# Optimization experiments

Hardware: AMD Instinct MI355X
Metric: run time of the kernel (lower is better)

## Reference

```python
import jax, jax.numpy as jnp
import numpy as np
from jax import lax

WINDOW_SIZE = 11
SIGMA = 1.5
LEVELS = 5
WEIGHTS = jnp.array([0.0448, 0.2856, 0.3001, 0.2363, 0.1333], dtype=jnp.float32)


def _make_window(ws, channel):
    # 1D gaussian, sigma=1.5, normalized; outer product -> 2D window, tiled per channel
    x = jnp.arange(ws, dtype=jnp.float32) - ws // 2
    g = jnp.exp(-(x * x) / (2.0 * SIGMA * SIGMA))
    g = g / g.sum()
    w2 = jnp.outer(g, g)  # [ws, ws]
    return jnp.broadcast_to(w2[None, None], (channel, 1, ws, ws))


def _dwconv(x, win, channel):
    # depthwise VALID conv, matches F.conv2d(..., padding=0, groups=channel)
    return lax.conv_general_dilated(
        x, win, window_strides=(1, 1), padding='VALID',
        feature_group_count=channel,
        dimension_numbers=('NCHW', 'OIHW', 'NCHW'))


def _ssim_cs(img1, img2):
    # dynamic data range, as in the torch source (L=1 for [0,1) inputs)
    max_val = jnp.where(jnp.max(img1) > 128.0, 255.0, 1.0)
    min_val = jnp.where(jnp.min(img1) < -0.5, -1.0, 0.0)
    L = max_val - min_val

    n, c, h, w = img1.shape
    ws = min(WINDOW_SIZE, h, w)  # static python int
    win = _make_window(ws, c)

    mu1 = _dwconv(img1, win, c)
    mu2 = _dwconv(img2, win, c)
    mu1_sq = mu1 * mu1
    mu2_sq = mu2 * mu2
    mu1_mu2 = mu1 * mu2
    sigma1_sq = _dwconv(img1 * img1, win, c) - mu1_sq
    sigma2_sq = _dwconv(img2 * img2, win, c) - mu2_sq
    sigma12 = _dwconv(img1 * img2, win, c) - mu1_mu2

    C1 = (0.01 * L) ** 2
    C2 = (0.03 * L) ** 2
    v1 = 2.0 * sigma12 + C2
    v2 = sigma1_sq + sigma2_sq + C2
    cs = jnp.mean(v1 / v2)
    ssim_map = (2.0 * mu1_mu2 + C1) * v1 / ((mu1_sq + mu2_sq + C1) * v2)
    return jnp.mean(ssim_map), cs


def _avg_pool2(x):
    # F.avg_pool2d(x, (2,2)): stride 2, no padding (floors odd dims)
    n, c, h, w = x.shape
    x = x[:, :, : (h // 2) * 2, : (w // 2) * 2]
    return x.reshape(n, c, h // 2, 2, w // 2, 2).mean(axis=(3, 5))


def setup_inputs() -> dict:
    key = jax.random.key(0)
    k1, k2 = jax.random.split(key)
    img1 = jax.random.uniform(k1, (16, 3, 512, 512), dtype=jnp.float32)
    img2 = jax.random.uniform(k2, (16, 3, 512, 512), dtype=jnp.float32)
    return {"img1": img1, "img2": img2}


def reference(img1, img2):
    mssim, mcs = [], []
    for _ in range(LEVELS):  # fixed 5-level pyramid, shapes shrink each level
        s, c = _ssim_cs(img1, img2)
        mssim.append(s)
        mcs.append(c)
        img1 = _avg_pool2(img1)
        img2 = _avg_pool2(img2)
    mssim = (jnp.stack(mssim) + 1.0) / 2.0  # normalize=True
    mcs = (jnp.stack(mcs) + 1.0) / 2.0
    pow1 = mcs ** WEIGHTS
    pow2 = mssim ** WEIGHTS
    # NOTE: faithful to source: prod over (pow1[:-1] * pow2[-1]) broadcasts pow2[-1]
    return jnp.prod(pow1[:-1] * pow2[-1])
```

## Files before the change

### kernel.cpp

```cpp
#include <hip/hip_runtime.h>


#define NSLOT 32

typedef float v4  __attribute__((ext_vector_type(4)));
typedef float v2f __attribute__((ext_vector_type(2)));
typedef _Float16 h4 __attribute__((ext_vector_type(4)));

__device__ __forceinline__ float frcp(float x) { return __builtin_amdgcn_rcpf(x); }

template<int TROWS, int NTHR, int MINW>
__global__ __launch_bounds__(NTHR, MINW) void ssim_tile_kernel(
    const float* __restrict__ img1, const float* __restrict__ img2,
    float* __restrict__ ds1, float* __restrict__ ds2,
    int H, int do_ds, float* __restrict__ acc)
{
    constexpr int HR    = TROWS + 10;
    constexpr int OPT   = TROWS * 32 / NTHR;
    constexpr int PITCH = 33;
    constexpr int NW    = NTHR / 64;

    const float GW[11] = {0.00102840f, 0.00759877f, 0.03600070f, 0.10936069f,
                          0.21300636f, 0.26601172f, 0.21300636f, 0.10936069f,
                          0.03600070f, 0.00759877f, 0.00102840f};
    const float C1 = 1e-4f, C2 = 9e-4f;

    __shared__ h4 hb[HR * PITCH];
    __shared__ float red[2 * NW];

    const int tid  = threadIdx.x;
    const int nc   = blockIdx.z;
    const int tx0  = blockIdx.x * 32;
    const int ty0  = blockIdx.y * TROWS;
    const int outHW = H - 10;
    const float* p1 = img1 + (size_t)nc * H * H;
    const float* p2 = img2 + (size_t)nc * H * H;

    if (do_ds) {
        const int H2 = H >> 1;
        #pragma unroll
        for (int t = tid; t < 16 * (TROWS / 2); t += NTHR) {
            int r = t >> 4, cdd = t & 15;
            int iy = ty0 + 2 * r, ix = tx0 + 2 * cdd;
            if (iy + 1 < H) {
                v2f a0 = *(const v2f*)(p1 + (size_t)iy * H + ix);
                v2f a1 = *(const v2f*)(p1 + (size_t)(iy + 1) * H + ix);
                v2f b0 = *(const v2f*)(p2 + (size_t)iy * H + ix);
                v2f b1 = *(const v2f*)(p2 + (size_t)(iy + 1) * H + ix);
                size_t o = (size_t)nc * H2 * H2
                         + (size_t)((ty0 >> 1) + r) * H2 + ((tx0 >> 1) + cdd);
                ds1[o] = 0.25f * ((a0.x + a0.y) + (a1.x + a1.y));
                ds2[o] = 0.25f * ((b0.x + b0.y) + (b1.x + b1.y));
            }
        }
    }

    for (int task = tid; task < HR * 8; task += NTHR) {
        const int r  = task >> 3, cg = task & 7;
        const int gr = ty0 + r;
        const int c0 = tx0 + cg * 4;
        v4 hs = 0.f, hd = 0.f, hss = 0.f, hdd = 0.f;
        if (gr < H) {
            float s[16], d[16];
            if (c0 + 16 <= H) {
                const float* pa = p1 + (size_t)gr * H + c0;
                const float* pb = p2 + (size_t)gr * H + c0;
                #pragma unroll
                for (int q = 0; q < 4; ++q) {
                    v4 va = *(const v4*)(pa + 4 * q);
                    v4 vb = *(const v4*)(pb + 4 * q);
                    v4 sv = va + vb, dv = va - vb;
                    s[4*q+0] = sv.x; s[4*q+1] = sv.y; s[4*q+2] = sv.z; s[4*q+3] = sv.w;
                    d[4*q+0] = dv.x; d[4*q+1] = dv.y; d[4*q+2] = dv.z; d[4*q+3] = dv.w;
                }
            } else {
                #pragma unroll
                for (int q = 0; q < 16; ++q) {
                    int cc = c0 + q;
                    float a = (cc < H) ? p1[(size_t)gr * H + cc] : 0.f;
                    float b = (cc < H) ? p2[(size_t)gr * H + cc] : 0.f;
                    s[q] = a + b; d[q] = a - b;
                }
            }
            #pragma unroll
            for (int j = 0; j < 11; ++j) {
                float w = GW[j];
                v4 sv = {s[j], s[j+1], s[j+2], s[j+3]};
                v4 dv = {d[j], d[j+1], d[j+2], d[j+3]};
                v4 ws = w * sv, wd = w * dv;
                hs += ws; hd += wd; hss += ws * sv; hdd += wd * dv;
            }
        }
        h4* row = &hb[r * PITCH + cg * 4];
        row[0] = (h4){(_Float16)hs.x, (_Float16)hd.x, (_Float16)hss.x, (_Float16)hdd.x};
        row[1] = (h4){(_Float16)hs.y, (_Float16)hd.y, (_Float16)hss.y, (_Float16)hdd.y};
        row[2] = (h4){(_Float16)hs.z, (_Float16)hd.z, (_Float16)hss.z, (_Float16)hdd.z};
        row[3] = (h4){(_Float16)hs.w, (_Float16)hd.w, (_Float16)hss.w, (_Float16)hdd.w};
    }
    __syncthreads();

    const int col  = tid & 31;
    const int row0 = (tid >> 5) * OPT;
    const float colm = (tx0 + col < outHW) ? 1.f : 0.f;
    v4 A[OPT];
    #pragma unroll
    for (int k = 0; k < OPT; ++k) A[k] = 0.f;

    #pragma unroll
    for (int r = 0; r < OPT + 10; ++r) {
        h4 h = hb[(row0 + r) * PITCH + col];
        v4 f = {(float)h.x, (float)h.y, (float)h.z, (float)h.w};
        #pragma unroll
        for (int k = 0; k < OPT; ++k) {
            const int j = r - k;
            if (j >= 0 && j < 11) A[k] += GW[j] * f;
        }
    }

    float ssim_t = 0.f, cs_t = 0.f;
    #pragma unroll
    for (int k = 0; k < OPT; ++k) {
        float mask = colm * ((ty0 + row0 + k < outHW) ? 1.f : 0.f);
        float mu_s = A[k].x, mu_d = A[k].y;
        float P = mu_s * mu_s, Q = mu_d * mu_d;
        float U = A[k].z - P, V = A[k].w - Q;
        float v1 = 0.5f * (U - V) + C2;
        float v2 = 0.5f * (U + V) + C2;
        float n1 = 0.5f * (P - Q) + C1;
        float d1 = 0.5f * (P + Q) + C1;
        float csv = v1 * frcp(v2);
        float ssv = n1 * csv * frcp(d1);
        cs_t   += mask * csv;
        ssim_t += mask * ssv;
    }

    #pragma unroll
    for (int off = 32; off > 0; off >>= 1) {
        ssim_t += __shfl_down(ssim_t, off);
        cs_t   += __shfl_down(cs_t, off);
    }
    int wave = tid >> 6, lane = tid & 63;
    if (lane == 0) { red[wave] = ssim_t; red[NW + wave] = cs_t; }
    __syncthreads();
    if (tid == 0) {
        float s = 0.f, c2s = 0.f;
        #pragma unroll
        for (int w = 0; w < NW; ++w) { s += red[w]; c2s += red[NW + w]; }
        int slot = (blockIdx.x + blockIdx.y * 5 + blockIdx.z * 11) & (NSLOT - 1);
        atomicAdd(&acc[slot], s);
        atomicAdd(&acc[NSLOT + slot], c2s);
    }
}

__global__ void finalize_kernel(const float* __restrict__ acc, float* __restrict__ out)
{
    if (threadIdx.x == 0 && blockIdx.x == 0) {
        const float w[5] = {0.0448f, 0.2856f, 0.3001f, 0.2363f, 0.1333f};
        float ms[5], mc[5];
        for (int l = 0; l < 5; ++l) {
            float s = 0.f, c = 0.f;
            for (int k = 0; k < NSLOT; ++k) {
                s += acc[2 * NSLOT * l + k];
                c += acc[2 * NSLOT * l + NSLOT + k];
            }
            int oh = (512 >> l) - 10;
            float cnt = 48.f * (float)oh * (float)oh;
            ms[l] = (s / cnt + 1.f) * 0.5f;
            mc[l] = (c / cnt + 1.f) * 0.5f;
        }
        float p2 = powf(ms[4], w[4]);
        float r = 1.f;
        for (int i = 0; i < 4; ++i) r *= powf(mc[i], w[i]) * p2;
        out[0] = r;
    }
}

extern "C" void kernel_launch(void* const* d_in, const int* in_sizes, int n_in,
                              void* d_out, int out_size, void* d_ws, size_t ws_size,
                              hipStream_t stream)
{
    const float* img1 = (const float*)d_in[0];
    const float* img2 = (const float*)d_in[1];
    float* out = (float*)d_out;
    float* ws  = (float*)d_ws;

    float* acc = ws;
    size_t off = 512;

    const float* buf1[5];
    const float* buf2[5];
    float* wbuf1[5];
    float* wbuf2[5];
    buf1[0] = img1; buf2[0] = img2;
    for (int l = 1; l < 5; ++l) {
        int Hl = 512 >> l;
        size_t sz = (size_t)48 * Hl * Hl;
        wbuf1[l] = ws + off; off += sz;
        wbuf2[l] = ws + off; off += sz;
        buf1[l] = wbuf1[l];
        buf2[l] = wbuf2[l];
    }

    hipMemsetAsync(acc, 0, 5 * 2 * NSLOT * sizeof(float), stream);

    const int Hs[5] = {512, 256, 128, 64, 32};
    const int Ts[5] = {64, 64, 32, 16, 16};

    for (int l = 0; l < 5; ++l) {
        int H = Hs[l], T = Ts[l];
        int outH = H - 10;
        int ctiles = (outH + 31) / 32;
        int rtiles = (outH + T - 1) / T;
        dim3 grid(ctiles, rtiles, 48);
        float* d1 = l < 4 ? wbuf1[l + 1] : nullptr;
        float* d2 = l < 4 ? wbuf2[l + 1] : nullptr;
        int dd = l < 4 ? 1 : 0;
        float* a = acc + 2 * NSLOT * l;
        if (T == 64)
            ssim_tile_kernel<64, 256, 8><<<grid, 256, 0, stream>>>(buf1[l], buf2[l], d1, d2, H, dd, a);
        else if (T == 32)
            ssim_tile_kernel<32, 256, 8><<<grid, 256, 0, stream>>>(buf1[l], buf2[l], d1, d2, H, dd, a);
        else
            ssim_tile_kernel<16, 256, 8><<<grid, 256, 0, stream>>>(buf1[l], buf2[l], d1, d2, H, dd, a);
    }

    finalize_kernel<<<1, 64, 0, stream>>>(acc, out);
}
```

Measured before the change: 253.2 us.

## Fuse all pyramid levels into one cooperative persistent kernel with grid syncs

Replaces the per-level kernel launches, memset and finalize launch with a single cooperative kernel that loops over tiles for each level and separates levels with grid-wide syncs. Accumulator zeroing and the final combine run inside the same kernel. This aims to remove launch gaps and tail effects between small levels, at the cost of grid sync overhead and occupancy capped by cooperative launch limits; the launch bounds also change from 8 to 4 minimum waves. A fallback path keeps separate launches if cooperative launch fails.

```diff
diff --git a/kernel.cpp b/kernel.cpp
--- a/kernel.cpp
+++ b/kernel.cpp
@@ -1,7 +1,10 @@
 #include <hip/hip_runtime.h>
+#include <hip/hip_cooperative_groups.h>
 
 
 #define NSLOT 32
+
+namespace cg = cooperative_groups;
 
 typedef float v4  __attribute__((ext_vector_type(4)));
 typedef float v2f __attribute__((ext_vector_type(2)));
@@ -9,29 +12,22 @@
 
 __device__ __forceinline__ float frcp(float x) { return __builtin_amdgcn_rcpf(x); }
 
-template<int TROWS, int NTHR, int MINW>
-__global__ __launch_bounds__(NTHR, MINW) void ssim_tile_kernel(
+template<int TROWS>
+__device__ __forceinline__ void ssim_tile(
     const float* __restrict__ img1, const float* __restrict__ img2,
     float* __restrict__ ds1, float* __restrict__ ds2,
-    int H, int do_ds, float* __restrict__ acc)
+    int H, int do_ds, float* __restrict__ acc,
+    int nc, int tx0, int ty0, h4* hb, float* red, int tid)
 {
     constexpr int HR    = TROWS + 10;
-    constexpr int OPT   = TROWS * 32 / NTHR;
+    constexpr int OPT   = TROWS * 32 / 256;
     constexpr int PITCH = 33;
-    constexpr int NW    = NTHR / 64;
 
     const float GW[11] = {0.00102840f, 0.00759877f, 0.03600070f, 0.10936069f,
                           0.21300636f, 0.26601172f, 0.21300636f, 0.10936069f,
                           0.03600070f, 0.00759877f, 0.00102840f};
     const float C1 = 1e-4f, C2 = 9e-4f;
 
-    __shared__ h4 hb[HR * PITCH];
-    __shared__ float red[2 * NW];
-
-    const int tid  = threadIdx.x;
-    const int nc   = blockIdx.z;
-    const int tx0  = blockIdx.x * 32;
-    const int ty0  = blockIdx.y * TROWS;
     const int outHW = H - 10;
     const float* p1 = img1 + (size_t)nc * H * H;
     const float* p2 = img2 + (size_t)nc * H * H;
@@ -39,7 +35,7 @@
     if (do_ds) {
         const int H2 = H >> 1;
         #pragma unroll
-        for (int t = tid; t < 16 * (TROWS / 2); t += NTHR) {
+        for (int t = tid; t < 16 * (TROWS / 2); t += 256) {
             int r = t >> 4, cdd = t & 15;
             int iy = ty0 + 2 * r, ix = tx0 + 2 * cdd;
             if (iy + 1 < H) {
@@ -55,10 +51,10 @@
         }
     }
 
-    for (int task = tid; task < HR * 8; task += NTHR) {
-        const int r  = task >> 3, cg = task & 7;
+    for (int task = tid; task < HR * 8; task += 256) {
+        const int r  = task >> 3, cg_ = task & 7;
         const int gr = ty0 + r;
-        const int c0 = tx0 + cg * 4;
+        const int c0 = tx0 + cg_ * 4;
         v4 hs = 0.f, hd = 0.f, hss = 0.f, hdd = 0.f;
         if (gr < H) {
             float s[16], d[16];
@@ -87,11 +83,11 @@
                 float w = GW[j];
                 v4 sv = {s[j], s[j+1], s[j+2], s[j+3]};
                 v4 dv = {d[j], d[j+1], d[j+2], d[j+3]};
-                v4 ws = w * sv, wd = w * dv;
-                hs += ws; hd += wd; hss += ws * sv; hdd += wd * dv;
+                v4 ws_ = w * sv, wd = w * dv;
+                hs += ws_; hd += wd; hss += ws_ * sv; hdd += wd * dv;
             }
         }
-        h4* row = &hb[r * PITCH + cg * 4];
+        h4* row = &hb[r * PITCH + cg_ * 4];
         row[0] = (h4){(_Float16)hs.x, (_Float16)hd.x, (_Float16)hss.x, (_Float16)hdd.x};
         row[1] = (h4){(_Float16)hs.y, (_Float16)hd.y, (_Float16)hss.y, (_Float16)hdd.y};
         row[2] = (h4){(_Float16)hs.z, (_Float16)hd.z, (_Float16)hss.z, (_Float16)hdd.z};
@@ -140,39 +136,117 @@
         cs_t   += __shfl_down(cs_t, off);
     }
     int wave = tid >> 6, lane = tid & 63;
-    if (lane == 0) { red[wave] = ssim_t; red[NW + wave] = cs_t; }
+    if (lane == 0) { red[wave] = ssim_t; red[4 + wave] = cs_t; }
     __syncthreads();
     if (tid == 0) {
-        float s = 0.f, c2s = 0.f;
-        #pragma unroll
-        for (int w = 0; w < NW; ++w) { s += red[w]; c2s += red[NW + w]; }
-        int slot = (blockIdx.x + blockIdx.y * 5 + blockIdx.z * 11) & (NSLOT - 1);
+        float s = red[0] + red[1] + red[2] + red[3];
+        float c2s = red[4] + red[5] + red[6] + red[7];
+        int slot = (tx0 + ty0 * 5 + nc * 11) & (NSLOT - 1);
         atomicAdd(&acc[slot], s);
         atomicAdd(&acc[NSLOT + slot], c2s);
     }
 }
 
+__device__ __forceinline__ void finalize_body(const float* __restrict__ acc,
+                                              float* __restrict__ out)
+{
+    const float w[5] = {0.0448f, 0.2856f, 0.3001f, 0.2363f, 0.1333f};
+    float ms[5], mc[5];
+    for (int l = 0; l < 5; ++l) {
+        float s = 0.f, c = 0.f;
+        for (int k = 0; k < NSLOT; ++k) {
+            s += acc[2 * NSLOT * l + k];
+            c += acc[2 * NSLOT * l + NSLOT + k];
+        }
+        int oh = (512 >> l) - 10;
+        float cnt = 48.f * (float)oh * (float)oh;
+        ms[l] = (s / cnt + 1.f) * 0.5f;
+        mc[l] = (c / cnt + 1.f) * 0.5f;
+    }
+    float p2 = powf(ms[4], w[4]);
+    float r = 1.f;
+    for (int i = 0; i < 4; ++i) r *= powf(mc[i], w[i]) * p2;
+    out[0] = r;
+}
+
+
+__global__ __launch_bounds__(256, 4) void ssim_all_kernel(
+    const float* __restrict__ img1, const float* __restrict__ img2,
+    float* __restrict__ ws, float* __restrict__ out)
+{
+    __shared__ h4 hb[74 * 33];
+    __shared__ float red[8];
+
+    const int tid = threadIdx.x;
+    const int bid = blockIdx.x;
+    const int nb  = gridDim.x;
+    cg::grid_group grid = cg::this_grid();
+
+    float* acc = ws;
+    float* l1a = ws + 512;      float* l1b = ws + 3146240;
+    float* l2a = ws + 6291968;  float* l2b = ws + 7078400;
+    float* l3a = ws + 7864832;  float* l3b = ws + 8061440;
+    float* l4a = ws + 8258048;  float* l4b = ws + 8307200;
+
+    if (bid == 0)
+        for (int i = tid; i < 2 * NSLOT * 5; i += 256) acc[i] = 0.f;
+    grid.sync();
+
+    for (int t = bid; t < 6144; t += nb) {
+        int nc = t >> 7, k = t & 127;
+        ssim_tile<64>(img1, img2, l1a, l1b, 512, 1, acc,
+                      nc, (k & 15) * 32, (k >> 4) * 64, hb, red, tid);
+    }
+    grid.sync();
+
+    for (int t = bid; t < 1536; t += nb) {
+        int nc = t >> 5, k = t & 31;
+        ssim_tile<64>(l1a, l1b, l2a, l2b, 256, 1, acc + 64,
+                      nc, (k & 7) * 32, (k >> 3) * 64, hb, red, tid);
+    }
+    grid.sync();
+
+    for (int t = bid; t < 768; t += nb) {
+        int nc = t >> 4, k = t & 15;
+        ssim_tile<32>(l2a, l2b, l3a, l3b, 128, 1, acc + 128,
+                      nc, (k & 3) * 32, (k >> 2) * 32, hb, red, tid);
+    }
+    grid.sync();
+
+    for (int t = bid; t < 384; t += nb) {
+        int nc = t >> 3, k = t & 7;
+        ssim_tile<16>(l3a, l3b, l4a, l4b, 64, 1, acc + 192,
+                      nc, (k & 1) * 32, (k >> 1) * 16, hb, red, tid);
+    }
+    grid.sync();
+
+    for (int t = bid; t < 96; t += nb) {
+        int nc = t >> 1, k = t & 1;
+        ssim_tile<16>(l4a, l4b, nullptr, nullptr, 32, 0, acc + 256,
+                      nc, 0, k * 16, hb, red, tid);
+    }
+    grid.sync();
+
+    if (bid == 0 && tid == 0) finalize_body(acc, out);
+}
+
+
+template<int TROWS>
+__global__ __launch_bounds__(256, 4) void ssim_level_kernel(
+    const float* __restrict__ img1, const float* __restrict__ img2,
+    float* __restrict__ ds1, float* __restrict__ ds2,
+    int H, int do_ds, float* __restrict__ acc)
+{
+    __shared__ h4 hb[(TROWS + 10) * 33];
+    __shared__ float red[8];
+    ssim_tile<TROWS>(img1, img2, ds1, ds2, H, do_ds, acc,
+                     blockIdx.z, blockIdx.x * 32, blockIdx.y * TROWS,
+                     hb, red, threadIdx.x);
+}
+
 __global__ void finalize_kernel(const float* __restrict__ acc, float* __restrict__ out)
 {
-    if (threadIdx.x == 0 && blockIdx.x == 0) {
-        const float w[5] = {0.0448f, 0.2856f, 0.3001f, 0.2363f, 0.1333f};
-        float ms[5], mc[5];
-        for (int l = 0; l < 5; ++l) {
-            float s = 0.f, c = 0.f;
-            for (int k = 0; k < NSLOT; ++k) {
-                s += acc[2 * NSLOT * l + k];
-                c += acc[2 * NSLOT * l + NSLOT + k];
-            }
-            int oh = (512 >> l) - 10;
-            float cnt = 48.f * (float)oh * (float)oh;
-            ms[l] = (s / cnt + 1.f) * 0.5f;
-            mc[l] = (c / cnt + 1.f) * 0.5f;
-        }
-        float p2 = powf(ms[4], w[4]);
-        float r = 1.f;
-        for (int i = 0; i < 4; ++i) r *= powf(mc[i], w[i]) * p2;
-        out[0] = r;
-    }
+    if (threadIdx.x == 0 && blockIdx.x == 0) finalize_body(acc, out);
 }
 
 extern "C" void kernel_launch(void* const* d_in, const int* in_sizes, int n_in,
@@ -184,45 +258,39 @@
     float* out = (float*)d_out;
     float* ws  = (float*)d_ws;
 
+    int bpc = 0;
+    hipError_t qerr = hipOccupancyMaxActiveBlocksPerMultiprocessor(
+        &bpc, ssim_all_kernel, 256, 0);
+    bool ok = false;
+    if (qerr == hipSuccess && bpc > 0) {
+        if (bpc > 8) bpc = 8;
+        int nblocks = bpc * 256;
+        if (nblocks > 6144) nblocks = 6144;
+        void* args[] = {(void*)&img1, (void*)&img2, (void*)&ws, (void*)&out};
+        hipError_t lerr = hipLaunchCooperativeKernel(
+            ssim_all_kernel, dim3(nblocks), dim3(256), args, 0, stream);
+        ok = (lerr == hipSuccess);
+    }
+    if (ok) return;
+
     float* acc = ws;
-    size_t off = 512;
-
-    const float* buf1[5];
-    const float* buf2[5];
-    float* wbuf1[5];
-    float* wbuf2[5];
-    buf1[0] = img1; buf2[0] = img2;
-    for (int l = 1; l < 5; ++l) {
-        int Hl = 512 >> l;
-        size_t sz = (size_t)48 * Hl * Hl;
-        wbuf1[l] = ws + off; off += sz;
-        wbuf2[l] = ws + off; off += sz;
-        buf1[l] = wbuf1[l];
-        buf2[l] = wbuf2[l];
-    }
+    float* l1a = ws + 512;      float* l1b = ws + 3146240;
+    float* l2a = ws + 6291968;  float* l2b = ws + 7078400;
+    float* l3a = ws + 7864832;  float* l3b = ws + 8061440;
+    float* l4a = ws + 8258048;  float* l4b = ws + 8307200;
 
     hipMemsetAsync(acc, 0, 5 * 2 * NSLOT * sizeof(float), stream);
 
-    const int Hs[5] = {512, 256, 128, 64, 32};
-    const int Ts[5] = {64, 64, 32, 16, 16};
-
-    for (int l = 0; l < 5; ++l) {
-        int H = Hs[l], T = Ts[l];
-        int outH = H - 10;
-        int ctiles = (outH + 31) / 32;
-        int rtiles = (outH + T - 1) / T;
-        dim3 grid(ctiles, rtiles, 48);
-        float* d1 = l < 4 ? wbuf1[l + 1] : nullptr;
-        float* d2 = l < 4 ? wbuf2[l + 1] : nullptr;
-        int dd = l < 4 ? 1 : 0;
-        float* a = acc + 2 * NSLOT * l;
-        if (T == 64)
-            ssim_tile_kernel<64, 256, 8><<<grid, 256, 0, stream>>>(buf1[l], buf2[l], d1, d2, H, dd, a);
-        else if (T == 32)
-            ssim_tile_kernel<32, 256, 8><<<grid, 256, 0, stream>>>(buf1[l], buf2[l], d1, d2, H, dd, a);
-        else
-            ssim_tile_kernel<16, 256, 8><<<grid, 256, 0, stream>>>(buf1[l], buf2[l], d1, d2, H, dd, a);
-    }
+    ssim_level_kernel<64><<<dim3(16, 8, 48), 256, 0, stream>>>(
+        img1, img2, l1a, l1b, 512, 1, acc);
+    ssim_level_kernel<64><<<dim3(8, 4, 48), 256, 0, stream>>>(
+        l1a, l1b, l2a, l2b, 256, 1, acc + 64);
+    ssim_level_kernel<32><<<dim3(4, 4, 48), 256, 0, stream>>>(
+        l2a, l2b, l3a, l3b, 128, 1, acc + 128);
+    ssim_level_kernel<16><<<dim3(2, 4, 48), 256, 0, stream>>>(
+        l3a, l3b, l4a, l4b, 64, 1, acc + 192);
+    ssim_level_kernel<16><<<dim3(1, 2, 48), 256, 0, stream>>>(
+        l4a, l4b, nullptr, nullptr, 32, 0, acc + 256);
 
     finalize_kernel<<<1, 64, 0, stream>>>(acc, out);
 }
```

After: 547.8 us. +116.4%, slower.
